# Optimization experiments

Measured on AMD Instinct MI355X. Metric: run time of the kernel, lower is better.

The kernel has to match this reference:

```python
import jax, jax.numpy as jnp
import numpy as np

B, S, D = 4, 1024, 1024
H = 16
DK = D // H  # per-head dim_q = dim_k = 64
DFF = 4096
EPS = 1e-5


def _layer_norm(x, g, b):
    m = jnp.mean(x, axis=-1, keepdims=True)
    v = jnp.mean((x - m) ** 2, axis=-1, keepdims=True)
    return (x - m) / jnp.sqrt(v + EPS) * g + b


def setup_inputs() -> dict:
    key = jax.random.key(0)
    ks = jax.random.split(key, 16)
    sd = 1.0 / np.sqrt(D)
    sk = 1.0 / np.sqrt(H * DK)
    sf = 1.0 / np.sqrt(DFF)
    return {
        "src": jax.random.normal(ks[0], (B, S, D), jnp.float32),
        # stacked per-head projections (torch loops over H separate nn.Linear)
        "Wq": jax.random.uniform(ks[1], (H, D, DK), jnp.float32, -sd, sd),
        "bq": jax.random.uniform(ks[2], (H, DK), jnp.float32, -sd, sd),
        "Wk": jax.random.uniform(ks[3], (H, D, DK), jnp.float32, -sd, sd),
        "bk": jax.random.uniform(ks[4], (H, DK), jnp.float32, -sd, sd),
        "Wv": jax.random.uniform(ks[5], (H, D, DK), jnp.float32, -sd, sd),
        "bv": jax.random.uniform(ks[6], (H, DK), jnp.float32, -sd, sd),
        "Wo": jax.random.uniform(ks[7], (H * DK, D), jnp.float32, -sk, sk),
        "bo": jax.random.uniform(ks[8], (D,), jnp.float32, -sk, sk),
        "g1": jnp.ones((D,), jnp.float32),
        "be1": jnp.zeros((D,), jnp.float32),
        "W1": jax.random.uniform(ks[9], (D, DFF), jnp.float32, -sd, sd),
        "b1": jax.random.uniform(ks[10], (DFF,), jnp.float32, -sd, sd),
        "W2": jax.random.uniform(ks[11], (DFF, D), jnp.float32, -sf, sf),
        "b2": jax.random.uniform(ks[12], (D,), jnp.float32, -sf, sf),
        "g2": jnp.ones((D,), jnp.float32),
        "be2": jnp.zeros((D,), jnp.float32),
    }


def reference(src, Wq, bq, Wk, bk, Wv, bv, Wo, bo, g1, be1, W1, b1, W2, b2, g2, be2):
    # multi-head attention (all heads batched via einsum instead of python loop)
    q = jnp.einsum("bsd,hdk->bhsk", src, Wq) + bq[None, :, None, :]
    k = jnp.einsum("bsd,hdk->bhsk", src, Wk) + bk[None, :, None, :]
    v = jnp.einsum("bsd,hdk->bhsk", src, Wv) + bv[None, :, None, :]
    scale = jnp.asarray(DK, src.dtype) ** 0.5  # query.size(-1) ** 0.5
    scores = jnp.einsum("bhsk,bhtk->bhst", q, k) / scale
    attn = jax.nn.softmax(scores, axis=-1)
    o = jnp.einsum("bhst,bhtk->bhsk", attn, v)  # [B,H,S,DK]
    o = o.transpose(0, 2, 1, 3).reshape(src.shape[0], src.shape[1], H * DK)
    attn_out = o @ Wo + bo
    x = _layer_norm(src + attn_out, g1, be1)
    ffn = jax.nn.relu(x @ W1 + b1) @ W2 + b2
    return _layer_norm(x + ffn, g2, be2)
```

## Files before the change

kernel.cpp:

```cpp
#include <hip/hip_runtime.h>
#include <hip/hip_bf16.h>

#define DEV __device__ __forceinline__

typedef __attribute__((ext_vector_type(8))) short bf16x8;
typedef __attribute__((ext_vector_type(4))) float f32x4;
typedef __attribute__((ext_vector_type(4))) short short4v;

DEV short f2bf(float f) {
    union { float f; unsigned u; } x; x.f = f;
    unsigned u = x.u;
    unsigned r = (u + 0x7fffu + ((u >> 16) & 1u)) >> 16;
    return (short)r;
}

DEV float bf2f(short s) {
    union { unsigned u; float f; } x;
    x.u = ((unsigned)(unsigned short)s) << 16;
    return x.f;
}

#define GLD16(g, l)                                                         \
    __builtin_amdgcn_global_load_lds(                                       \
        (const __attribute__((address_space(1))) void*)(g),                 \
        (__attribute__((address_space(3))) void*)(l), 16, 0, 0)

#define WAITV(n) asm volatile("s_waitcnt vmcnt(" #n ")" ::: "memory")
#define SBAR()   asm volatile("s_barrier" ::: "memory")
#define LGKM0()                                              \
    asm volatile("s_waitcnt lgkmcnt(0)" ::: "memory");       \
    __builtin_amdgcn_sched_barrier(0)


__global__ __launch_bounds__(256) void k_cast(const float* __restrict__ in,
                                              short* __restrict__ out, int n4) {
    int i = blockIdx.x * 256 + threadIdx.x;
    if (i >= n4) return;
    float4 v = ((const float4*)in)[i];
    short4v o;
    o[0] = f2bf(v.x); o[1] = f2bf(v.y); o[2] = f2bf(v.z); o[3] = f2bf(v.w);
    ((short4v*)out)[i] = o;
}

__global__ __launch_bounds__(256) void k_tr(const float* __restrict__ in,
                                            short* __restrict__ out,
                                            int R, int C,
                                            long in_hs, long out_hs) {
    in  += (size_t)blockIdx.z * in_hs;
    out += (size_t)blockIdx.z * out_hs;
    __shared__ short tile[64][68];
    const int t = threadIdx.x;
    const int r0 = blockIdx.y * 64, c0 = blockIdx.x * 64;
    const int lr = t >> 4, lc4 = (t & 15) * 4;
#pragma unroll
    for (int it = 0; it < 4; ++it) {
        int r = lr + it * 16;
        float4 v = *(const float4*)(in + (size_t)(r0 + r) * C + c0 + lc4);
        tile[lc4 + 0][r] = f2bf(v.x);
        tile[lc4 + 1][r] = f2bf(v.y);
        tile[lc4 + 2][r] = f2bf(v.z);
        tile[lc4 + 3][r] = f2bf(v.w);
    }
    __syncthreads();
#pragma unroll
    for (int it = 0; it < 4; ++it) {
        int c = lr + it * 16;
        short4v o;
        o[0] = tile[c][lc4 + 0];
        o[1] = tile[c][lc4 + 1];
        o[2] = tile[c][lc4 + 2];
        o[3] = tile[c][lc4 + 3];
        *(short4v*)(out + (size_t)(c0 + c) * R + r0 + lc4) = o;
    }
}

template <int MODE>
__global__ __launch_bounds__(512, 2) void k_gemm8(
    const short* __restrict__ A, const short* __restrict__ BT,
    int K, int NT,
    const float* __restrict__ f0, const float* __restrict__ f1,
    const float* __restrict__ f2,
    void* __restrict__ o0, void* __restrict__ o1, void* __restrict__ o2) {
    __shared__ short lds[2][2][2][128 * 64];
    const int t = threadIdx.x;
    const int w = t >> 6, l = t & 63;
    const int l16 = l & 15, lg = l >> 4;
    const int wm = w >> 2, wn = w & 3;
    const int bn = blockIdx.x, bm = blockIdx.y;
    const int koff = blockIdx.z * NT * 64;
    const short* Ab = A + (size_t)bm * 256 * K + koff;
    const short* Bb = BT + (size_t)bn * 256 * K + koff;
    const int srow = l >> 3;
    const int scol = ((l & 7) ^ srow) * 8;
    const int offk0 = ((0 + lg) ^ (l16 & 7)) * 8;
    const int offk1 = ((4 + lg) ^ (l16 & 7)) * 8;

    f32x4 acc[8][4] = {};

    auto stg = [&](int buf, int op, int h, int kt) {
#pragma unroll
        for (int i = 0; i < 2; ++i) {
            int row = h * 128 + w * 16 + i * 8 + srow;
            GLD16((op ? Bb : Ab) + (size_t)row * K + (size_t)kt * 64 + scol,
                  &lds[buf][op][h][(w * 16 + i * 8) * 64]);
        }
    };

    stg(0, 0, 0, 0); stg(0, 0, 1, 0);
    stg(0, 1, 0, 0); stg(0, 1, 1, 0);
    const int t1p = (NT > 1) ? 1 : 0;
    stg(1, 1, 0, t1p); stg(1, 1, 1, t1p);
    WAITV(4);
    SBAR();

    for (int kt = 0; kt < NT; ++kt) {
        const int cur = kt & 1, nxt = cur ^ 1;
        const int t1 = (kt + 1 < NT) ? kt + 1 : NT - 1;
        const int t2 = (kt + 2 < NT) ? kt + 2 : NT - 1;
        bf16x8 a0[4][2], a1[4][2], b0[2][2], b1[2][2];

#pragma unroll
        for (int m = 0; m < 4; ++m) {
            a0[m][0] = *(const bf16x8*)&lds[cur][0][wm][(m * 16 + l16) * 64 + offk0];
            a0[m][1] = *(const bf16x8*)&lds[cur][0][wm][(m * 16 + l16) * 64 + offk1];
        }
#pragma unroll
        for (int n = 0; n < 2; ++n) {
            int r = (wn & 1) * 64 + n * 16 + l16;
            b0[n][0] = *(const bf16x8*)&lds[cur][1][wn >> 1][r * 64 + offk0];
            b0[n][1] = *(const bf16x8*)&lds[cur][1][wn >> 1][r * 64 + offk1];
        }
        stg(nxt, 0, 0, t1);
        SBAR();
        LGKM0();
        __builtin_amdgcn_s_setprio(1);
#pragma unroll
        for (int m = 0; m < 4; ++m)
#pragma unroll
            for (int n = 0; n < 2; ++n) {
                acc[m][n] = __builtin_amdgcn_mfma_f32_16x16x32_bf16(a0[m][0], b0[n][0], acc[m][n], 0, 0, 0);
                acc[m][n] = __builtin_amdgcn_mfma_f32_16x16x32_bf16(a0[m][1], b0[n][1], acc[m][n], 0, 0, 0);
            }
        __builtin_amdgcn_s_setprio(0);
        SBAR();

#pragma unroll
        for (int n = 0; n < 2; ++n) {
            int r = (wn & 1) * 64 + (n + 2) * 16 + l16;
            b1[n][0] = *(const bf16x8*)&lds[cur][1][wn >> 1][r * 64 + offk0];
            b1[n][1] = *(const bf16x8*)&lds[cur][1][wn >> 1][r * 64 + offk1];
        }
        stg(nxt, 0, 1, t1);
        SBAR();
        LGKM0();
        __builtin_amdgcn_s_setprio(1);
#pragma unroll
        for (int m = 0; m < 4; ++m)
#pragma unroll
            for (int n = 0; n < 2; ++n) {
                acc[m][n + 2] = __builtin_amdgcn_mfma_f32_16x16x32_bf16(a0[m][0], b1[n][0], acc[m][n + 2], 0, 0, 0);
                acc[m][n + 2] = __builtin_amdgcn_mfma_f32_16x16x32_bf16(a0[m][1], b1[n][1], acc[m][n + 2], 0, 0, 0);
            }
        __builtin_amdgcn_s_setprio(0);
        SBAR();

#pragma unroll
        for (int m = 0; m < 4; ++m) {
            a1[m][0] = *(const bf16x8*)&lds[cur][0][wm][((m + 4) * 16 + l16) * 64 + offk0];
            a1[m][1] = *(const bf16x8*)&lds[cur][0][wm][((m + 4) * 16 + l16) * 64 + offk1];
        }
        stg(cur, 1, 0, t2);
        SBAR();
        LGKM0();
        __builtin_amdgcn_s_setprio(1);
#pragma unroll
        for (int m = 0; m < 4; ++m)
#pragma unroll
            for (int n = 0; n < 2; ++n) {
                acc[m + 4][n + 2] = __builtin_amdgcn_mfma_f32_16x16x32_bf16(a1[m][0], b1[n][0], acc[m + 4][n + 2], 0, 0, 0);
                acc[m + 4][n + 2] = __builtin_amdgcn_mfma_f32_16x16x32_bf16(a1[m][1], b1[n][1], acc[m + 4][n + 2], 0, 0, 0);
            }
        __builtin_amdgcn_s_setprio(0);
        SBAR();

        stg(cur, 1, 1, t2);
        SBAR();
        __builtin_amdgcn_s_setprio(1);
#pragma unroll
        for (int m = 0; m < 4; ++m)
#pragma unroll
            for (int n = 0; n < 2; ++n) {
                acc[m + 4][n] = __builtin_amdgcn_mfma_f32_16x16x32_bf16(a1[m][0], b0[n][0], acc[m + 4][n], 0, 0, 0);
                acc[m + 4][n] = __builtin_amdgcn_mfma_f32_16x16x32_bf16(a1[m][1], b0[n][1], acc[m + 4][n], 0, 0, 0);
            }
        __builtin_amdgcn_s_setprio(0);
        WAITV(4);
        SBAR();
    }
    WAITV(0);

    const int N = gridDim.x * 256;
#pragma unroll
    for (int m = 0; m < 8; ++m) {
        int rowbase = bm * 256 + wm * 128 + m * 16 + lg * 4;
#pragma unroll
        for (int n = 0; n < 4; ++n) {
            int col = bn * 256 + wn * 64 + n * 16 + l16;
            if constexpr (MODE == 0) {
                int p = col >> 10, c1 = col & 1023;
                int hh = c1 >> 6, dk = c1 & 63;
                const float* bias = (p == 0) ? f0 : (p == 1) ? f1 : f2;
                float bvl = bias[c1];
                int b = rowbase >> 10, s = rowbase & 1023;
                if (p == 2) {
                    short4v vv;
#pragma unroll
                    for (int rr = 0; rr < 4; ++rr) vv[rr] = f2bf(acc[m][n][rr] + bvl);
                    *(short4v*)((short*)o2 + (((size_t)(b * 16 + hh) * 64 + dk) << 10) + s) = vv;
                } else {
                    short* dst = (p == 0) ? (short*)o0 : (short*)o1;
#pragma unroll
                    for (int rr = 0; rr < 4; ++rr)
                        dst[(((size_t)(b * 16 + hh) << 10) + s + rr) * 64 + dk] =
                            f2bf(acc[m][n][rr] + bvl);
                }
            } else if constexpr (MODE == 2) {
                float bvl = f0[col];
#pragma unroll
                for (int rr = 0; rr < 4; ++rr) {
                    size_t idx = (size_t)(rowbase + rr) * N + col;
                    float y = acc[m][n][rr] + bvl;
                    ((short*)o0)[idx] = f2bf(y > 0.f ? y : 0.f);
                }
            } else {
                size_t base =
                    ((size_t)blockIdx.z * (gridDim.y * 256) + rowbase) * N + col;
#pragma unroll
                for (int rr = 0; rr < 4; ++rr)
                    ((short*)o0)[base + (size_t)rr * N] = f2bf(acc[m][n][rr]);
            }
        }
    }
}

__global__ __launch_bounds__(256) void k_gemm_s(
    const short* __restrict__ A, const short* __restrict__ BT, int K,
    const float* __restrict__ f0, const float* __restrict__ resid,
    float* __restrict__ o0) {
    __shared__ short Al[128][72];
    __shared__ short Bl[128][72];
    const int t = threadIdx.x;
    const int l = t & 63, w = t >> 6;
    const int l16 = l & 15, lg = l >> 4;
    const int wm = w >> 1, wn = w & 1;
    const int bn = blockIdx.x, bm = blockIdx.y;
    f32x4 acc[4][4] = {};
    const short* Ab = A + (size_t)bm * 128 * K;
    const short* Bb = BT + (size_t)bn * 128 * K;
    const int sr = t >> 3, sc = (t & 7) * 8;

    for (int k0 = 0; k0 < K; k0 += 64) {
#pragma unroll
        for (int it = 0; it < 4; ++it) {
            int rr = sr + it * 32;
            *(bf16x8*)&Al[rr][sc] = *(const bf16x8*)(Ab + (size_t)rr * K + k0 + sc);
            *(bf16x8*)&Bl[rr][sc] = *(const bf16x8*)(Bb + (size_t)rr * K + k0 + sc);
        }
        __syncthreads();
#pragma unroll
        for (int kk = 0; kk < 2; ++kk) {
            bf16x8 af[4], bfv[4];
#pragma unroll
            for (int i = 0; i < 4; ++i)
                af[i] = *(const bf16x8*)&Al[wm * 64 + i * 16 + l16][kk * 32 + lg * 8];
#pragma unroll
            for (int j = 0; j < 4; ++j)
                bfv[j] = *(const bf16x8*)&Bl[wn * 64 + j * 16 + l16][kk * 32 + lg * 8];
#pragma unroll
            for (int i = 0; i < 4; ++i)
#pragma unroll
                for (int j = 0; j < 4; ++j)
                    acc[i][j] = __builtin_amdgcn_mfma_f32_16x16x32_bf16(
                        af[i], bfv[j], acc[i][j], 0, 0, 0);
        }
        __syncthreads();
    }

    const int N = gridDim.x * 128;
#pragma unroll
    for (int i = 0; i < 4; ++i) {
#pragma unroll
        for (int rr = 0; rr < 4; ++rr) {
            int row = bm * 128 + wm * 64 + i * 16 + lg * 4 + rr;
#pragma unroll
            for (int j = 0; j < 4; ++j) {
                int col = bn * 128 + wn * 64 + j * 16 + l16;
                size_t idx = (size_t)row * N + col;
                o0[idx] = acc[i][j][rr] + f0[col] + resid[idx];
            }
        }
    }
}

__global__ __launch_bounds__(256, 4) void k_attn(const short* __restrict__ Q,
                                                 const short* __restrict__ Kt,
                                                 const short* __restrict__ VT,
                                                 short* __restrict__ O) {
    __shared__ short Kl[2][64 * 64];
    __shared__ short Vl[2][64 * 64];
    __shared__ short Pl[4][16 * 64];
    const int bh = blockIdx.x;
    const int qb = blockIdx.y;
    const int t = threadIdx.x;
    const int w = t >> 6, l = t & 63;
    const int l16 = l & 15, lg = l >> 4;
    const int srow = l >> 3, scol = (l & 7) * 8;

    const short* Qb = Q + ((size_t)bh * 1024 + qb * 64 + w * 16 + l16) * 64 + lg * 8;
    bf16x8 qf0 = *(const bf16x8*)Qb;
    bf16x8 qf1 = *(const bf16x8*)(Qb + 32);

    const short* Kbase = Kt + (size_t)bh * (1024 * 64);
    const short* Vbase = VT + (size_t)bh * (64 * 1024);

    float m[4] = {-1e30f, -1e30f, -1e30f, -1e30f};
    float ls[4] = {0.f, 0.f, 0.f, 0.f};
    f32x4 oacc[4] = {};

    auto stage = [&](int buf, int t0) {
#pragma unroll
        for (int it = 0; it < 2; ++it) {
            int roww = w * 16 + it * 8;
            GLD16(Kbase + (size_t)(t0 + roww + srow) * 64 + scol,
                  &Kl[buf][roww * 64]);
            GLD16(Vbase + (size_t)(roww + srow) * 1024 + t0 + scol,
                  &Vl[buf][roww * 64]);
        }
    };

    auto compute = [&](int cur) {
        f32x4 s[4];
#pragma unroll
        for (int n = 0; n < 4; ++n) {
            bf16x8 kf0 = *(const bf16x8*)&Kl[cur][(n * 16 + l16) * 64 + lg * 8];
            bf16x8 kf1 = *(const bf16x8*)&Kl[cur][(n * 16 + l16) * 64 + 32 + lg * 8];
            f32x4 a = {0.f, 0.f, 0.f, 0.f};
            a = __builtin_amdgcn_mfma_f32_16x16x32_bf16(qf0, kf0, a, 0, 0, 0);
            a = __builtin_amdgcn_mfma_f32_16x16x32_bf16(qf1, kf1, a, 0, 0, 0);
            s[n] = a * 0.125f;
        }
#pragma unroll
        for (int r = 0; r < 4; ++r) {
            float mx = fmaxf(fmaxf(s[0][r], s[1][r]), fmaxf(s[2][r], s[3][r]));
            mx = fmaxf(mx, __shfl_xor(mx, 1));
            mx = fmaxf(mx, __shfl_xor(mx, 2));
            mx = fmaxf(mx, __shfl_xor(mx, 4));
            mx = fmaxf(mx, __shfl_xor(mx, 8));
            float mn = fmaxf(m[r], mx);
            float al = __expf(m[r] - mn);
            m[r] = mn;
            float su = 0.f;
#pragma unroll
            for (int n = 0; n < 4; ++n) {
                float p = __expf(s[n][r] - mn);
                s[n][r] = p;
                su += p;
            }
            su += __shfl_xor(su, 1);
            su += __shfl_xor(su, 2);
            su += __shfl_xor(su, 4);
            su += __shfl_xor(su, 8);
            ls[r] = ls[r] * al + su;
#pragma unroll
            for (int n = 0; n < 4; ++n) oacc[n][r] *= al;
        }
#pragma unroll
        for (int n = 0; n < 4; ++n)
#pragma unroll
            for (int r = 0; r < 4; ++r) {
                int prow = lg * 4 + r;
                int pch = (n * 2 + (l16 >> 3)) ^ (prow & 7);
                Pl[w][prow * 64 + pch * 8 + (l16 & 7)] = f2bf(s[n][r]);
            }
#pragma unroll
        for (int n = 0; n < 4; ++n) {
#pragma unroll
            for (int kk = 0; kk < 2; ++kk) {
                int rch = (kk * 4 + lg) ^ (l16 & 7);
                bf16x8 pa = *(const bf16x8*)&Pl[w][l16 * 64 + rch * 8];
                bf16x8 vb = *(const bf16x8*)&Vl[cur][(n * 16 + l16) * 64 +
                                                     kk * 32 + lg * 8];
                oacc[n] = __builtin_amdgcn_mfma_f32_16x16x32_bf16(pa, vb, oacc[n],
                                                                  0, 0, 0);
            }
        }
    };

    stage(0, 0);
    for (int ti = 0; ti < 15; ++ti) {
        int cur = ti & 1;
        stage(cur ^ 1, (ti + 1) * 64);
        WAITV(4);
        SBAR();
        compute(cur);
        SBAR();
    }
    WAITV(0);
    SBAR();
    compute(1);

    const int b = bh >> 4, h = bh & 15;
#pragma unroll
    for (int r = 0; r < 4; ++r) {
        float inv = 1.f / ls[r];
        size_t row = (size_t)(b * 1024 + qb * 64 + w * 16 + lg * 4 + r);
#pragma unroll
        for (int n = 0; n < 4; ++n)
            O[row * 1024 + h * 64 + n * 16 + l16] = f2bf(oacc[n][r] * inv);
    }
}

__global__ __launch_bounds__(256) void k_ln(const float* __restrict__ in,
                                            const float* __restrict__ g,
                                            const float* __restrict__ be,
                                            float* __restrict__ of,
                                            short* __restrict__ ob) {
    const int row = blockIdx.x, t = threadIdx.x;
    float4 x = ((const float4*)(in + ((size_t)row << 10)))[t];
    float s = x.x + x.y + x.z + x.w;
    float s2 = x.x * x.x + x.y * x.y + x.z * x.z + x.w * x.w;
#pragma unroll
    for (int mm = 1; mm < 64; mm <<= 1) {
        s += __shfl_xor(s, mm);
        s2 += __shfl_xor(s2, mm);
    }
    __shared__ float red[8];
    if ((t & 63) == 0) { red[t >> 6] = s; red[4 + (t >> 6)] = s2; }
    __syncthreads();
    s = red[0] + red[1] + red[2] + red[3];
    s2 = red[4] + red[5] + red[6] + red[7];
    float mean = s * (1.f / 1024.f);
    float var = s2 * (1.f / 1024.f) - mean * mean;
    float rstd = rsqrtf(var + 1e-5f);
    int c = t * 4;
    float4 y;
    y.x = (x.x - mean) * rstd * g[c + 0] + be[c + 0];
    y.y = (x.y - mean) * rstd * g[c + 1] + be[c + 1];
    y.z = (x.z - mean) * rstd * g[c + 2] + be[c + 2];
    y.w = (x.w - mean) * rstd * g[c + 3] + be[c + 3];
    if (of) ((float4*)(of + ((size_t)row << 10)))[t] = y;
    if (ob) {
        short4v o;
        o[0] = f2bf(y.x); o[1] = f2bf(y.y); o[2] = f2bf(y.z); o[3] = f2bf(y.w);
        ((short4v*)(ob + ((size_t)row << 10)))[t] = o;
    }
}

__global__ __launch_bounds__(256) void k_lnred(const short* __restrict__ part,
                                               const float* __restrict__ bias,
                                               const float* __restrict__ resid,
                                               const float* __restrict__ g,
                                               const float* __restrict__ be,
                                               float* __restrict__ of) {
    const int row = blockIdx.x, t = threadIdx.x;
    float4 x = ((const float4*)(resid + ((size_t)row << 10)))[t];
    float4 bv = ((const float4*)bias)[t];
    x.x += bv.x; x.y += bv.y; x.z += bv.z; x.w += bv.w;
#pragma unroll
    for (int kz = 0; kz < 4; ++kz) {
        short4v p = ((const short4v*)(part + (((size_t)kz * 4096 + row) << 10)))[t];
        x.x += bf2f(p[0]); x.y += bf2f(p[1]); x.z += bf2f(p[2]); x.w += bf2f(p[3]);
    }
    float s = x.x + x.y + x.z + x.w;
    float s2 = x.x * x.x + x.y * x.y + x.z * x.z + x.w * x.w;
#pragma unroll
    for (int mm = 1; mm < 64; mm <<= 1) {
        s += __shfl_xor(s, mm);
        s2 += __shfl_xor(s2, mm);
    }
    __shared__ float red[8];
    if ((t & 63) == 0) { red[t >> 6] = s; red[4 + (t >> 6)] = s2; }
    __syncthreads();
    s = red[0] + red[1] + red[2] + red[3];
    s2 = red[4] + red[5] + red[6] + red[7];
    float mean = s * (1.f / 1024.f);
    float var = s2 * (1.f / 1024.f) - mean * mean;
    float rstd = rsqrtf(var + 1e-5f);
    int c = t * 4;
    float4 y;
    y.x = (x.x - mean) * rstd * g[c + 0] + be[c + 0];
    y.y = (x.y - mean) * rstd * g[c + 1] + be[c + 1];
    y.z = (x.z - mean) * rstd * g[c + 2] + be[c + 2];
    y.w = (x.w - mean) * rstd * g[c + 3] + be[c + 3];
    ((float4*)(of + ((size_t)row << 10)))[t] = y;
}

extern "C" void kernel_launch(void* const* d_in, const int* in_sizes, int n_in,
                              void* d_out, int out_size, void* d_ws, size_t ws_size,
                              hipStream_t stream) {
    (void)in_sizes; (void)n_in; (void)out_size; (void)ws_size;
    const float* src = (const float*)d_in[0];
    const float* Wq  = (const float*)d_in[1];
    const float* bq  = (const float*)d_in[2];
    const float* Wk  = (const float*)d_in[3];
    const float* bk  = (const float*)d_in[4];
    const float* Wv  = (const float*)d_in[5];
    const float* bv  = (const float*)d_in[6];
    const float* Wo  = (const float*)d_in[7];
    const float* bo  = (const float*)d_in[8];
    const float* g1  = (const float*)d_in[9];
    const float* be1 = (const float*)d_in[10];
    const float* W1  = (const float*)d_in[11];
    const float* b1  = (const float*)d_in[12];
    const float* W2  = (const float*)d_in[13];
    const float* b2  = (const float*)d_in[14];
    const float* g2  = (const float*)d_in[15];
    const float* be2 = (const float*)d_in[16];

    char* ws = (char*)d_ws;
    const size_t MB = 1048576;
    short* srcbf = (short*)(ws + 0);
    short* Qb    = (short*)(ws + 8 * MB);
    short* Kb    = (short*)(ws + 16 * MB);
    short* VTb   = (short*)(ws + 24 * MB);
    short* h1    = (short*)(ws + 0);
    short* Obuf  = srcbf;
    short* W2T   = (short*)(ws + 32 * MB);
    float* xf    = (float*)(ws + 40 * MB);
    short* WqkvT = (short*)(ws + 56 * MB);
    short* WoT   = (short*)(ws + 62 * MB);
    short* W1T   = (short*)(ws + 64 * MB);
    float* xres  = (float*)(ws + 72 * MB);
    short* xbf   = (short*)(ws + 88 * MB);
    short* part  = (short*)(ws + 56 * MB);

    k_cast<<<4096, 256, 0, stream>>>(src, srcbf, 1048576);
    k_tr<<<dim3(1, 16, 16), 256, 0, stream>>>(Wq, WqkvT,           1024, 64, 65536, 65536);
    k_tr<<<dim3(1, 16, 16), 256, 0, stream>>>(Wk, WqkvT + 1048576, 1024, 64, 65536, 65536);
    k_tr<<<dim3(1, 16, 16), 256, 0, stream>>>(Wv, WqkvT + 2097152, 1024, 64, 65536, 65536);
    k_tr<<<dim3(16, 16, 1), 256, 0, stream>>>(Wo, WoT, 1024, 1024, 0, 0);
    k_tr<<<dim3(64, 16, 1), 256, 0, stream>>>(W1, W1T, 1024, 4096, 0, 0);
    k_tr<<<dim3(16, 64, 1), 256, 0, stream>>>(W2, W2T, 4096, 1024, 0, 0);
    k_gemm8<0><<<dim3(12, 16, 1), 512, 0, stream>>>(srcbf, WqkvT, 1024, 16,
                                                    bq, bk, bv, Qb, Kb, VTb);
    k_attn<<<dim3(64, 16), 256, 0, stream>>>(Qb, Kb, VTb, Obuf);
    k_gemm_s<<<dim3(8, 32), 256, 0, stream>>>(Obuf, WoT, 1024, bo, src, xres);
    k_ln<<<4096, 256, 0, stream>>>(xres, g1, be1, xf, xbf);
    k_gemm8<2><<<dim3(16, 16, 1), 512, 0, stream>>>(xbf, W1T, 1024, 16,
                                                    b1, nullptr, nullptr,
                                                    h1, nullptr, nullptr);
    k_gemm8<3><<<dim3(4, 16, 4), 512, 0, stream>>>(h1, W2T, 4096, 16,
                                                   nullptr, nullptr, nullptr,
                                                   part, nullptr, nullptr);
    k_lnred<<<4096, 256, 0, stream>>>(part, b2, xf, g2, be2, (float*)d_out);
}
```

Measured before the change: 249.6 us.

## Swizzle K/V LDS tiles, use exp2 softmax with lazy max rescaling

```diff
diff --git a/kernel.cpp b/kernel.cpp
--- a/kernel.cpp
+++ b/kernel.cpp
@@ -314,7 +314,9 @@
     const int t = threadIdx.x;
     const int w = t >> 6, l = t & 63;
     const int l16 = l & 15, lg = l >> 4;
-    const int srow = l >> 3, scol = (l & 7) * 8;
+    const int sw = l16 & 7;
+    const int srow = l >> 3;
+    const int scol = ((l & 7) ^ srow) * 8;
 
     const short* Qb = Q + ((size_t)bh * 1024 + qb * 64 + w * 16 + l16) * 64 + lg * 8;
     bf16x8 qf0 = *(const bf16x8*)Qb;
@@ -322,6 +324,9 @@
 
     const short* Kbase = Kt + (size_t)bh * (1024 * 64);
     const short* Vbase = VT + (size_t)bh * (64 * 1024);
+
+    const float SCALE = 0.125f * 1.44269504089f;
+    const float THR = 11.5415603f;
 
     float m[4] = {-1e30f, -1e30f, -1e30f, -1e30f};
     float ls[4] = {0.f, 0.f, 0.f, 0.f};
@@ -342,13 +347,15 @@
         f32x4 s[4];
 #pragma unroll
         for (int n = 0; n < 4; ++n) {
-            bf16x8 kf0 = *(const bf16x8*)&Kl[cur][(n * 16 + l16) * 64 + lg * 8];
-            bf16x8 kf1 = *(const bf16x8*)&Kl[cur][(n * 16 + l16) * 64 + 32 + lg * 8];
+            bf16x8 kf0 = *(const bf16x8*)&Kl[cur][(n * 16 + l16) * 64 + (lg ^ sw) * 8];
+            bf16x8 kf1 = *(const bf16x8*)&Kl[cur][(n * 16 + l16) * 64 + ((4 + lg) ^ sw) * 8];
             f32x4 a = {0.f, 0.f, 0.f, 0.f};
             a = __builtin_amdgcn_mfma_f32_16x16x32_bf16(qf0, kf0, a, 0, 0, 0);
             a = __builtin_amdgcn_mfma_f32_16x16x32_bf16(qf1, kf1, a, 0, 0, 0);
-            s[n] = a * 0.125f;
-        }
+            s[n] = a * SCALE;
+        }
+        float mx4[4];
+        bool need = false;
 #pragma unroll
         for (int r = 0; r < 4; ++r) {
             float mx = fmaxf(fmaxf(s[0][r], s[1][r]), fmaxf(s[2][r], s[3][r]));
@@ -356,23 +363,46 @@
             mx = fmaxf(mx, __shfl_xor(mx, 2));
             mx = fmaxf(mx, __shfl_xor(mx, 4));
             mx = fmaxf(mx, __shfl_xor(mx, 8));
-            float mn = fmaxf(m[r], mx);
-            float al = __expf(m[r] - mn);
-            m[r] = mn;
-            float su = 0.f;
-#pragma unroll
-            for (int n = 0; n < 4; ++n) {
-                float p = __expf(s[n][r] - mn);
-                s[n][r] = p;
-                su += p;
-            }
-            su += __shfl_xor(su, 1);
-            su += __shfl_xor(su, 2);
-            su += __shfl_xor(su, 4);
-            su += __shfl_xor(su, 8);
-            ls[r] = ls[r] * al + su;
-#pragma unroll
-            for (int n = 0; n < 4; ++n) oacc[n][r] *= al;
+            mx4[r] = mx;
+            need = need || (mx > m[r] + THR);
+        }
+        if (__any(need)) {
+#pragma unroll
+            for (int r = 0; r < 4; ++r) {
+                float mn = fmaxf(m[r], mx4[r]);
+                float al = exp2f(m[r] - mn);
+                m[r] = mn;
+                float su = 0.f;
+#pragma unroll
+                for (int n = 0; n < 4; ++n) {
+                    float p = exp2f(s[n][r] - mn);
+                    s[n][r] = p;
+                    su += p;
+                }
+                su += __shfl_xor(su, 1);
+                su += __shfl_xor(su, 2);
+                su += __shfl_xor(su, 4);
+                su += __shfl_xor(su, 8);
+                ls[r] = ls[r] * al + su;
+#pragma unroll
+                for (int n = 0; n < 4; ++n) oacc[n][r] *= al;
+            }
+        } else {
+#pragma unroll
+            for (int r = 0; r < 4; ++r) {
+                float su = 0.f;
+#pragma unroll
+                for (int n = 0; n < 4; ++n) {
+                    float p = exp2f(s[n][r] - m[r]);
+                    s[n][r] = p;
+                    su += p;
+                }
+                su += __shfl_xor(su, 1);
+                su += __shfl_xor(su, 2);
+                su += __shfl_xor(su, 4);
+                su += __shfl_xor(su, 8);
+                ls[r] += su;
+            }
         }
 #pragma unroll
         for (int n = 0; n < 4; ++n)
@@ -386,10 +416,9 @@
         for (int n = 0; n < 4; ++n) {
 #pragma unroll
             for (int kk = 0; kk < 2; ++kk) {
-                int rch = (kk * 4 + lg) ^ (l16 & 7);
-                bf16x8 pa = *(const bf16x8*)&Pl[w][l16 * 64 + rch * 8];
-                bf16x8 vb = *(const bf16x8*)&Vl[cur][(n * 16 + l16) * 64 +
-                                                     kk * 32 + lg * 8];
+                int rch = (kk * 4 + lg) ^ sw;
+                bf16x8 pa = *(const bf16x8*)&Pl[w][l16 * 64 + ((kk * 4 + lg) ^ sw) * 8];
+                bf16x8 vb = *(const bf16x8*)&Vl[cur][(n * 16 + l16) * 64 + rch * 8];
                 oacc[n] = __builtin_amdgcn_mfma_f32_16x16x32_bf16(pa, vb, oacc[n],
                                                                   0, 0, 0);
             }
```

After: 238.0 us. 4.6% less time.

## Restructure attention softmax: transposed scores, exp2 with prescaled Q, lazy rescale, swizzled LDS

Applied to the files above, without the earlier changes.

```diff
diff --git a/kernel.cpp b/kernel.cpp
--- a/kernel.cpp
+++ b/kernel.cpp
@@ -6,6 +6,7 @@
 typedef __attribute__((ext_vector_type(8))) short bf16x8;
 typedef __attribute__((ext_vector_type(4))) float f32x4;
 typedef __attribute__((ext_vector_type(4))) short short4v;
+typedef __attribute__((ext_vector_type(2))) unsigned uint2v;
 
 DEV short f2bf(float f) {
     union { float f; unsigned u; } x; x.f = f;
@@ -18,6 +19,12 @@
     union { unsigned u; float f; } x;
     x.u = ((unsigned)(unsigned short)s) << 16;
     return x.f;
+}
+
+DEV unsigned cvtpk(float a, float b) {
+    unsigned r;
+    asm("v_cvt_pk_bf16_f32 %0, %1, %2" : "=v"(r) : "v"(a), "v"(b));
+    return r;
 }
 
 #define GLD16(g, l)                                                         \
@@ -211,6 +218,7 @@
                 int hh = c1 >> 6, dk = c1 & 63;
                 const float* bias = (p == 0) ? f0 : (p == 1) ? f1 : f2;
                 float bvl = bias[c1];
+                float qs = (p == 0) ? 0.18033688011112042f : 1.0f;
                 int b = rowbase >> 10, s = rowbase & 1023;
                 if (p == 2) {
                     short4v vv;
@@ -222,7 +230,7 @@
 #pragma unroll
                     for (int rr = 0; rr < 4; ++rr)
                         dst[(((size_t)(b * 16 + hh) << 10) + s + rr) * 64 + dk] =
-                            f2bf(acc[m][n][rr] + bvl);
+                            f2bf((acc[m][n][rr] + bvl) * qs);
                 }
             } else if constexpr (MODE == 2) {
                 float bvl = f0[col];
@@ -314,7 +322,10 @@
     const int t = threadIdx.x;
     const int w = t >> 6, l = t & 63;
     const int l16 = l & 15, lg = l >> 4;
-    const int srow = l >> 3, scol = (l & 7) * 8;
+    const int sw = l16 & 7;
+    const int pmask = (l16 & 7) << 1;
+    const int srow = l >> 3;
+    const int scol = ((l & 7) ^ srow) * 8;
 
     const short* Qb = Q + ((size_t)bh * 1024 + qb * 64 + w * 16 + l16) * 64 + lg * 8;
     bf16x8 qf0 = *(const bf16x8*)Qb;
@@ -323,8 +334,9 @@
     const short* Kbase = Kt + (size_t)bh * (1024 * 64);
     const short* Vbase = VT + (size_t)bh * (64 * 1024);
 
-    float m[4] = {-1e30f, -1e30f, -1e30f, -1e30f};
-    float ls[4] = {0.f, 0.f, 0.f, 0.f};
+    const float THR = 11.5415603f;
+
+    float m = -1e30f, ls = 0.f;
     f32x4 oacc[4] = {};
 
     auto stage = [&](int buf, int t0) {
@@ -342,54 +354,71 @@
         f32x4 s[4];
 #pragma unroll
         for (int n = 0; n < 4; ++n) {
-            bf16x8 kf0 = *(const bf16x8*)&Kl[cur][(n * 16 + l16) * 64 + lg * 8];
-            bf16x8 kf1 = *(const bf16x8*)&Kl[cur][(n * 16 + l16) * 64 + 32 + lg * 8];
+            bf16x8 kf0 = *(const bf16x8*)&Kl[cur][(n * 16 + l16) * 64 + (lg ^ sw) * 8];
+            bf16x8 kf1 = *(const bf16x8*)&Kl[cur][(n * 16 + l16) * 64 + ((4 + lg) ^ sw) * 8];
             f32x4 a = {0.f, 0.f, 0.f, 0.f};
-            a = __builtin_amdgcn_mfma_f32_16x16x32_bf16(qf0, kf0, a, 0, 0, 0);
-            a = __builtin_amdgcn_mfma_f32_16x16x32_bf16(qf1, kf1, a, 0, 0, 0);
-            s[n] = a * 0.125f;
-        }
-#pragma unroll
-        for (int r = 0; r < 4; ++r) {
-            float mx = fmaxf(fmaxf(s[0][r], s[1][r]), fmaxf(s[2][r], s[3][r]));
-            mx = fmaxf(mx, __shfl_xor(mx, 1));
-            mx = fmaxf(mx, __shfl_xor(mx, 2));
-            mx = fmaxf(mx, __shfl_xor(mx, 4));
-            mx = fmaxf(mx, __shfl_xor(mx, 8));
-            float mn = fmaxf(m[r], mx);
-            float al = __expf(m[r] - mn);
-            m[r] = mn;
-            float su = 0.f;
+            a = __builtin_amdgcn_mfma_f32_16x16x32_bf16(kf0, qf0, a, 0, 0, 0);
+            a = __builtin_amdgcn_mfma_f32_16x16x32_bf16(kf1, qf1, a, 0, 0, 0);
+            s[n] = a;
+        }
+        float t0m = fmaxf(fmaxf(s[0][0], s[0][1]), fmaxf(s[0][2], s[0][3]));
+        float t1m = fmaxf(fmaxf(s[1][0], s[1][1]), fmaxf(s[1][2], s[1][3]));
+        float t2m = fmaxf(fmaxf(s[2][0], s[2][1]), fmaxf(s[2][2], s[2][3]));
+        float t3m = fmaxf(fmaxf(s[3][0], s[3][1]), fmaxf(s[3][2], s[3][3]));
+        float mx = fmaxf(fmaxf(t0m, t1m), fmaxf(t2m, t3m));
+        mx = fmaxf(mx, __shfl_xor(mx, 16));
+        mx = fmaxf(mx, __shfl_xor(mx, 32));
+
+        if (__any(mx > m + THR)) {
+            float mn = fmaxf(m, mx);
+            float al = exp2f(m - mn);
+            m = mn;
+#pragma unroll
+            for (int n = 0; n < 4; ++n)
+#pragma unroll
+                for (int r = 0; r < 4; ++r) s[n][r] = exp2f(s[n][r] - m);
+            float su = (s[0][0] + s[0][1]) + (s[0][2] + s[0][3]);
+            su += (s[1][0] + s[1][1]) + (s[1][2] + s[1][3]);
+            su += (s[2][0] + s[2][1]) + (s[2][2] + s[2][3]);
+            su += (s[3][0] + s[3][1]) + (s[3][2] + s[3][3]);
+            su += __shfl_xor(su, 16);
+            su += __shfl_xor(su, 32);
+            ls = ls * al + su;
+#pragma unroll
+            for (int r = 0; r < 4; ++r) {
+                float alr = __shfl(al, lg * 4 + r);
+#pragma unroll
+                for (int n = 0; n < 4; ++n) oacc[n][r] *= alr;
+            }
+        } else {
+#pragma unroll
+            for (int n = 0; n < 4; ++n)
+#pragma unroll
+                for (int r = 0; r < 4; ++r) s[n][r] = exp2f(s[n][r] - m);
+            float su = (s[0][0] + s[0][1]) + (s[0][2] + s[0][3]);
+            su += (s[1][0] + s[1][1]) + (s[1][2] + s[1][3]);
+            su += (s[2][0] + s[2][1]) + (s[2][2] + s[2][3]);
+            su += (s[3][0] + s[3][1]) + (s[3][2] + s[3][3]);
+            su += __shfl_xor(su, 16);
+            su += __shfl_xor(su, 32);
+            ls += su;
+        }
+#pragma unroll
+        for (int n = 0; n < 4; ++n) {
+            uint2v pv;
+            pv[0] = cvtpk(s[n][0], s[n][1]);
+            pv[1] = cvtpk(s[n][2], s[n][3]);
+            int g = (n * 4 + lg) ^ pmask;
+            *(uint2v*)((char*)Pl[w] + l16 * 128 + g * 8) = pv;
+        }
+#pragma unroll
+        for (int kk = 0; kk < 2; ++kk) {
+            int gp = (8 * kk + 2 * lg) ^ pmask;
+            bf16x8 pa = *(const bf16x8*)((const char*)Pl[w] + l16 * 128 + gp * 8);
 #pragma unroll
             for (int n = 0; n < 4; ++n) {
-                float p = __expf(s[n][r] - mn);
-                s[n][r] = p;
-                su += p;
-            }
-            su += __shfl_xor(su, 1);
-            su += __shfl_xor(su, 2);
-            su += __shfl_xor(su, 4);
-            su += __shfl_xor(su, 8);
-            ls[r] = ls[r] * al + su;
-#pragma unroll
-            for (int n = 0; n < 4; ++n) oacc[n][r] *= al;
-        }
-#pragma unroll
-        for (int n = 0; n < 4; ++n)
-#pragma unroll
-            for (int r = 0; r < 4; ++r) {
-                int prow = lg * 4 + r;
-                int pch = (n * 2 + (l16 >> 3)) ^ (prow & 7);
-                Pl[w][prow * 64 + pch * 8 + (l16 & 7)] = f2bf(s[n][r]);
-            }
-#pragma unroll
-        for (int n = 0; n < 4; ++n) {
-#pragma unroll
-            for (int kk = 0; kk < 2; ++kk) {
-                int rch = (kk * 4 + lg) ^ (l16 & 7);
-                bf16x8 pa = *(const bf16x8*)&Pl[w][l16 * 64 + rch * 8];
                 bf16x8 vb = *(const bf16x8*)&Vl[cur][(n * 16 + l16) * 64 +
-                                                     kk * 32 + lg * 8];
+                                                     ((kk * 4 + lg) ^ sw) * 8];
                 oacc[n] = __builtin_amdgcn_mfma_f32_16x16x32_bf16(pa, vb, oacc[n],
                                                                   0, 0, 0);
             }
@@ -412,7 +441,8 @@
     const int b = bh >> 4, h = bh & 15;
 #pragma unroll
     for (int r = 0; r < 4; ++r) {
-        float inv = 1.f / ls[r];
+        float lsr = __shfl(ls, lg * 4 + r);
+        float inv = 1.f / lsr;
         size_t row = (size_t)(b * 1024 + qb * 64 + w * 16 + lg * 4 + r);
 #pragma unroll
         for (int n = 0; n < 4; ++n)
```

New measurement: 219.6 us. -12.0%, faster.
